# Kernel optimization log

Measured on AMD Instinct MI355X. Metric: run time of the kernel, lower is better.

Reference implementation:

```python
import jax, jax.numpy as jnp
import numpy as np

B, T, M, D, H, DH = 2, 2048, 2048, 384, 4, 96
NM, DF, R, NA = 8, 1536, 16, 4
S = 0.02  # weight init scale

PARAM_NAMES = ['cWq','cbq','cWk','cbk','cWv','cbv','cWo','cbo',
               'sWq','sbq','sWk','sbk','sWv','sbv','sWo','sbo',
               'gW','gb','f1W','f1b','f2W','f2b','adA','adB',
               'ln1g','ln1b','ln2g','ln2b','ln3g','ln3b']

def setup_inputs() -> dict:
    key = jax.random.key(0)
    ks = jax.random.split(key, 20)
    n = lambda k, sh, s=1.0: jax.random.normal(k, sh, dtype=jnp.float32) * s
    z = lambda sh: jnp.zeros(sh, dtype=jnp.float32)
    o = lambda sh: jnp.ones(sh, dtype=jnp.float32)
    return {
        'x': n(ks[0], (B, T, D)),
        'mem': n(ks[1], (B, M, D)),
        'motif_ctrl': n(ks[2], (B, NM)),
        'adapter_idx': 1,
        'cWq': n(ks[3], (D, D), S), 'cbq': z((D,)),
        'cWk': n(ks[4], (D, D), S), 'cbk': z((D,)),
        'cWv': n(ks[5], (D, D), S), 'cbv': z((D,)),
        'cWo': n(ks[6], (D, D), S), 'cbo': z((D,)),
        'sWq': n(ks[7], (D, D), S), 'sbq': z((D,)),
        'sWk': n(ks[8], (D, D), S), 'sbk': z((D,)),
        'sWv': n(ks[9], (D, D), S), 'sbv': z((D,)),
        'sWo': n(ks[10], (D, D), S), 'sbo': z((D,)),
        'gW': n(ks[11], (H, NM), S), 'gb': z((H,)),
        'f1W': n(ks[12], (DF, D), S), 'f1b': z((DF,)),
        'f2W': n(ks[13], (D, DF), S), 'f2b': z((D,)),
        'adA': n(ks[14], (NA, R, D), S),
        'adB': n(ks[15], (NA, D, R), S),
        'ln1g': o((D,)), 'ln1b': z((D,)),
        'ln2g': o((D,)), 'ln2b': z((D,)),
        'ln3g': o((D,)), 'ln3b': z((D,)),
    }

def _lin(x, W, b):
    return x @ W.T + b  # torch nn.Linear convention: W is [out, in]

def _layernorm(x, g, b):
    mu = x.mean(-1, keepdims=True)
    var = ((x - mu) ** 2).mean(-1, keepdims=True)
    return (x - mu) * jax.lax.rsqrt(var + 1e-5) * g + b

def _block(x, mem, motif_ctrl, adapter_idx, p):
    scale = 1.0 / np.sqrt(DH).astype(np.float32)
    # --- cross-attention over memory ---
    h = _layernorm(x, p['ln1g'], p['ln1b'])
    q = _lin(h, p['cWq'], p['cbq']).reshape(B, T, H, DH)
    k = _lin(mem, p['cWk'], p['cbk']).reshape(B, M, H, DH)
    v = _lin(mem, p['cWv'], p['cbv']).reshape(B, M, H, DH)
    A = jax.nn.softmax(jnp.einsum('bthd,bmhd->bhtm', q, k) * scale, axis=-1)
    z = jnp.einsum('bhtm,bmhd->bthd', A, v).reshape(B, T, D)
    x = x + _lin(z, p['cWo'], p['cbo'])
    # --- motif-gated self-attention (post-softmax per-head gate) ---
    h = _layernorm(x, p['ln2g'], p['ln2b'])
    gates = jax.nn.sigmoid(motif_ctrl @ p['gW'].T + p['gb'])  # [B, H]
    q = _lin(h, p['sWq'], p['sbq']).reshape(B, T, H, DH)
    k = _lin(h, p['sWk'], p['sbk']).reshape(B, T, H, DH)
    v = _lin(h, p['sWv'], p['sbv']).reshape(B, T, H, DH)
    A = jax.nn.softmax(jnp.einsum('bthd,bshd->bhts', q, k) * scale, axis=-1)
    A = A * gates[:, :, None, None]
    z = jnp.einsum('bhts,bshd->bthd', A, v).reshape(B, T, D)
    x = x + _lin(z, p['sWo'], p['sbo'])
    # --- LoRA-adapter FFN ---
    h = _layernorm(x, p['ln3g'], p['ln3b'])
    f = _lin(jax.nn.gelu(_lin(h, p['f1W'], p['f1b']), approximate=False), p['f2W'], p['f2b'])
    f = f + (h @ p['adA'][adapter_idx].T) @ p['adB'][adapter_idx].T
    return x + f

def reference(x, mem, motif_ctrl, adapter_idx,
              cWq, cbq, cWk, cbk, cWv, cbv, cWo, cbo,
              sWq, sbq, sWk, sbk, sWv, sbv, sWo, sbo,
              gW, gb, f1W, f1b, f2W, f2b, adA, adB,
              ln1g, ln1b, ln2g, ln2b, ln3g, ln3b):
    p = dict(zip(PARAM_NAMES, (cWq, cbq, cWk, cbk, cWv, cbv, cWo, cbo,
                               sWq, sbq, sWk, sbk, sWv, sbv, sWo, sbo,
                               gW, gb, f1W, f1b, f2W, f2b, adA, adB,
                               ln1g, ln1b, ln2g, ln2b, ln3g, ln3b)))
    return _block(x, mem, motif_ctrl, int(adapter_idx), p)
```

## Files before the change

kernel.cpp:

```cpp
#include <hip/hip_runtime.h>
#include <hip/hip_bf16.h>
#include <math.h>

#define B_   2
#define T_   2048
#define M_   2048
#define D_   384
#define H_   4
#define DH_  96
#define NM_  8
#define DF_  1536
#define R_   16
#define NR_  4096

typedef unsigned short u16;
typedef u16    u16x8  __attribute__((ext_vector_type(8)));
typedef u16    u16x4  __attribute__((ext_vector_type(4)));
typedef __bf16 bf16x8 __attribute__((ext_vector_type(8)));
typedef float  f32x4  __attribute__((ext_vector_type(4)));

union V8 { u16x8 u; bf16x8 b; };
__device__ __forceinline__ bf16x8 as_bf(u16x8 x) { V8 v; v.u = x; return v.b; }

__device__ __forceinline__ u16 f2bf(float f) {
    unsigned u = __float_as_uint(f);
    unsigned r = (u + 0x7fffu + ((u >> 16) & 1u)) >> 16;
    return (u16)r;
}

__device__ __forceinline__ void load16(const u16* g, u16* l) {
    __builtin_amdgcn_global_load_lds(
        (const __attribute__((address_space(1))) void*)g,
        (__attribute__((address_space(3))) void*)l, 16, 0, 0);
}

__global__ __launch_bounds__(256)
void setup_kernel(const float* cWq, const float* cWk, const float* cWv, const float* cWo,
                  const float* sWq, const float* sWk, const float* sWv, const float* sWo,
                  const float* f1W, const float* f2W, const float* adA, const float* adB,
                  const float* mem,
                  u16* Wq_c, u16* Wkv_c, u16* Wco, u16* Wqkv_s, u16* Wso,
                  u16* Wf1, u16* Wf2, u16* WadA, u16* WadB, u16* memb,
                  const float* cbk, const float* cbv,
                  const float* sbq, const float* sbk, const float* sbv,
                  float* bkv_c, float* bqkv_s,
                  const float* mc, const float* gW, const float* gb, float* gates) {
    int seg = blockIdx.y;
    if (seg == 13) {
        for (int i = blockIdx.x * 256 + threadIdx.x; i < 1928; i += gridDim.x * 256) {
            if (i < 768) bkv_c[i] = (i < 384) ? cbk[i] : cbv[i - 384];
            else if (i < 1920) {
                int j = i - 768;
                bqkv_s[j] = (j < 384) ? sbq[j] : (j < 768 ? sbk[j - 384] : sbv[j - 768]);
            } else {
                int k = i - 1920;
                int b = k / H_, h = k % H_;
                float s = gb[h];
                for (int n = 0; n < NM_; n++)
                    s += mc[b * NM_ + n] * gW[h * NM_ + n];
                gates[k] = 1.f / (1.f + __expf(-s));
            }
        }
        return;
    }
    const float* s; u16* d; int n;
    switch (seg) {
        case 0:  s = cWq; d = Wq_c;            n = 147456; break;
        case 1:  s = cWk; d = Wkv_c;           n = 147456; break;
        case 2:  s = cWv; d = Wkv_c + 147456;  n = 147456; break;
        case 3:  s = cWo; d = Wco;             n = 147456; break;
        case 4:  s = sWq; d = Wqkv_s;          n = 147456; break;
        case 5:  s = sWk; d = Wqkv_s + 147456; n = 147456; break;
        case 6:  s = sWv; d = Wqkv_s + 294912; n = 147456; break;
        case 7:  s = sWo; d = Wso;             n = 147456; break;
        case 8:  s = f1W; d = Wf1;             n = 589824; break;
        case 9:  s = f2W; d = Wf2;             n = 589824; break;
        case 10: s = adA; d = WadA;            n = 24576;  break;
        case 11: s = adB; d = WadB;            n = 24576;  break;
        default: s = mem; d = memb;            n = 1572864; break;
    }
    for (int i = blockIdx.x * 256 + threadIdx.x; i < n; i += gridDim.x * 256)
        d[i] = f2bf(s[i]);
}

__global__ __launch_bounds__(384)
void ln_kernel(const float* __restrict__ x, const float* __restrict__ g,
               const float* __restrict__ b, u16* __restrict__ out) {
    __shared__ float sm[8];
    int row = blockIdx.x;
    int t = threadIdx.x;
    float v = x[(long)row * D_ + t];

    float s = v;
    for (int o = 32; o > 0; o >>= 1) s += __shfl_down(s, o);
    if ((t & 63) == 0) sm[t >> 6] = s;
    __syncthreads();
    float mu = 0.f;
    for (int i = 0; i < 6; i++) mu += sm[i];
    mu *= (1.f / D_);
    __syncthreads();

    float d = v - mu;
    s = d * d;
    for (int o = 32; o > 0; o >>= 1) s += __shfl_down(s, o);
    if ((t & 63) == 0) sm[t >> 6] = s;
    __syncthreads();
    float var = 0.f;
    for (int i = 0; i < 6; i++) var += sm[i];
    var *= (1.f / D_);

    float r = rsqrtf(var + 1e-5f);
    out[(long)row * D_ + t] = f2bf(d * r * g[t] + b[t]);
}

template<int ACT, bool OBF, bool VT, bool LORA>
__global__ __launch_bounds__(256)
void gemm_pipe(const u16* __restrict__ A, const u16* __restrict__ W,
               const float* __restrict__ bias, const float* __restrict__ res,
               void* __restrict__ Cout, int NC, int K,
               u16* __restrict__ Vt, int vtbase,
               const u16* __restrict__ Tl, const u16* __restrict__ adB,
               const int* __restrict__ aidx) {
    __shared__ __align__(16) u16 As[8192];
    __shared__ __align__(16) u16 Ws[8192];
    int tid = threadIdx.x, w = tid >> 6, lane = tid & 63;
    int l15 = lane & 15, quad = lane >> 4;
    int bm = blockIdx.y * 64, bn = blockIdx.x * 64;
    int mt0 = (w & 1) * 2, nt0 = (w >> 1) * 2;

    const u16* Ag[2]; const u16* Wg[2]; u16* Al[2]; u16* Wl[2];
    #pragma unroll
    for (int s = 0; s < 2; s++) {
        int r = s * 4 + w, mt = r >> 1, kc = r & 1;
        Ag[s] = A + (long)(bm + mt * 16 + l15) * K + kc * 32 + quad * 8;
        Wg[s] = W + (long)(bn + mt * 16 + l15) * K + kc * 32 + quad * 8;
        Al[s] = As + r * 512;
        Wl[s] = Ws + r * 512;
    }

    f32x4 acc[2][2];
    #pragma unroll
    for (int i = 0; i < 2; i++)
        #pragma unroll
        for (int j = 0; j < 2; j++) acc[i][j] = (f32x4){0.f, 0.f, 0.f, 0.f};

    int niter = K >> 6;
    #pragma unroll
    for (int s = 0; s < 2; s++) { load16(Ag[s], Al[s]); load16(Wg[s], Wl[s]); }

    for (int i = 0; i < niter; i++) {
        __syncthreads();
        int cur = (i & 1) * 4096, nxt = 4096 - cur;
        if (i + 1 < niter) {
            int k = (i + 1) << 6;
            #pragma unroll
            for (int s = 0; s < 2; s++) {
                load16(Ag[s] + k, Al[s] + nxt);
                load16(Wg[s] + k, Wl[s] + nxt);
            }
        }
        #pragma unroll
        for (int kc = 0; kc < 2; kc++) {
            u16x8 af[2], bfv[2];
            #pragma unroll
            for (int s = 0; s < 2; s++) {
                af[s]  = *(const u16x8*)(As + cur + ((mt0 + s) * 2 + kc) * 512 + lane * 8);
                bfv[s] = *(const u16x8*)(Ws + cur + ((nt0 + s) * 2 + kc) * 512 + lane * 8);
            }
            #pragma unroll
            for (int s = 0; s < 2; s++)
                #pragma unroll
                for (int j = 0; j < 2; j++)
                    acc[s][j] = __builtin_amdgcn_mfma_f32_16x16x32_bf16(
                        as_bf(af[s]), as_bf(bfv[j]), acc[s][j], 0, 0, 0);
        }
    }

    if (LORA) {
        long aoff = (long)aidx[0] * 6144;
        u16x8 tlf[2] = {{0,0,0,0,0,0,0,0}, {0,0,0,0,0,0,0,0}};
        u16x8 adf[2] = {{0,0,0,0,0,0,0,0}, {0,0,0,0,0,0,0,0}};
        #pragma unroll
        for (int s = 0; s < 2; s++) {
            if (quad < 2) {
                tlf[s] = *(const u16x8*)(Tl + (long)(bm + (mt0 + s) * 16 + l15) * 16 + quad * 8);
                adf[s] = *(const u16x8*)(adB + aoff + (long)(bn + (nt0 + s) * 16 + l15) * 16 + quad * 8);
            }
        }
        #pragma unroll
        for (int s = 0; s < 2; s++)
            #pragma unroll
            for (int j = 0; j < 2; j++)
                acc[s][j] = __builtin_amdgcn_mfma_f32_16x16x32_bf16(
                    as_bf(tlf[s]), as_bf(adf[j]), acc[s][j], 0, 0, 0);
    }

    #pragma unroll
    for (int mi = 0; mi < 2; mi++) {
        #pragma unroll
        for (int nj = 0; nj < 2; nj++) {
            int col = bn + (nt0 + nj) * 16 + l15;
            float bv = bias ? bias[col] : 0.f;
            int rowb = bm + (mt0 + mi) * 16 + quad * 4;
            if (VT && col >= vtbase) {
                int vc = col - vtbase;
                int b = rowb >> 11, rowl = rowb & 2047;
                u16x4 ov;
                #pragma unroll
                for (int r = 0; r < 4; r++) ov[r] = f2bf(acc[mi][nj][r] + bv);
                *(u16x4*)(Vt + ((long)b * 384 + vc) * 2048 + rowl) = ov;
            } else {
                #pragma unroll
                for (int r = 0; r < 4; r++) {
                    float v = acc[mi][nj][r] + bv;
                    if (ACT == 1) v = 0.5f * v * (1.f + erff(v * 0.70710678118654752f));
                    long idx = (long)(rowb + r) * NC + col;
                    if (res) v += res[idx];
                    if (OBF) ((u16*)Cout)[idx] = f2bf(v);
                    else     ((float*)Cout)[idx] = v;
                }
            }
        }
    }
}

template<int ACT, bool OBF>
__global__ __launch_bounds__(256)
void gemm_small(const u16* __restrict__ A, const u16* __restrict__ W,
                const float* __restrict__ bias, const float* __restrict__ res,
                void* __restrict__ Cout, int NR, int NC, int K,
                const int* __restrict__ aidx, int astride) {
    if (aidx) W += (long)aidx[0] * astride;
    __shared__ __align__(16) u16 As[2048];
    __shared__ __align__(16) u16 Ws[2048];
    int tid = threadIdx.x;
    int w = tid >> 6, lane = tid & 63;
    int bm = blockIdx.y * 64, bn = blockIdx.x * 64;
    int mt0 = (w & 1) * 2, nt0 = (w >> 1) * 2;

    int srow = ((tid >> 6) << 4) + (tid & 15);
    int kq8  = ((tid >> 4) & 3) * 8;
    const u16* Ag = A + (long)(bm + srow) * K + kq8;
    int wrow = bn + srow;
    const u16* Wg = W + (long)wrow * K + kq8;
    bool wok = wrow < NC;

    f32x4 acc[2][2];
    #pragma unroll
    for (int i = 0; i < 2; i++)
        #pragma unroll
        for (int j = 0; j < 2; j++) acc[i][j] = (f32x4){0.f, 0.f, 0.f, 0.f};

    for (int k0 = 0; k0 < K; k0 += 32) {
        u16x8 av = {0, 0, 0, 0, 0, 0, 0, 0};
        u16x8 wv = {0, 0, 0, 0, 0, 0, 0, 0};
        bool kok = (k0 + kq8) < K;
        if (kok) av = *(const u16x8*)(Ag + k0);
        if (kok && wok) wv = *(const u16x8*)(Wg + k0);
        __syncthreads();
        *(u16x8*)(As + tid * 8) = av;
        *(u16x8*)(Ws + tid * 8) = wv;
        __syncthreads();
        u16x8 af[2], bfv[2];
        #pragma unroll
        for (int i = 0; i < 2; i++) {
            af[i]  = *(const u16x8*)(As + (mt0 + i) * 512 + lane * 8);
            bfv[i] = *(const u16x8*)(Ws + (nt0 + i) * 512 + lane * 8);
        }
        #pragma unroll
        for (int i = 0; i < 2; i++)
            #pragma unroll
            for (int j = 0; j < 2; j++)
                acc[i][j] = __builtin_amdgcn_mfma_f32_16x16x32_bf16(
                    as_bf(af[i]), as_bf(bfv[j]), acc[i][j], 0, 0, 0);
    }

    int quad = lane >> 4, l15 = lane & 15;
    #pragma unroll
    for (int mi = 0; mi < 2; mi++) {
        #pragma unroll
        for (int nj = 0; nj < 2; nj++) {
            int col = bn + (nt0 + nj) * 16 + l15;
            if (col < NC) {
                float bv = bias ? bias[col] : 0.f;
                int rowb = bm + (mt0 + mi) * 16 + quad * 4;
                #pragma unroll
                for (int r = 0; r < 4; r++) {
                    float v = acc[mi][nj][r] + bv;
                    if (ACT == 1) v = 0.5f * v * (1.f + erff(v * 0.70710678118654752f));
                    long idx = (long)(rowb + r) * NC + col;
                    if (res) v += res[idx];
                    if (OBF) ((u16*)Cout)[idx] = f2bf(v);
                    else     ((float*)Cout)[idx] = v;
                }
            }
        }
    }
}

__global__ __launch_bounds__(256)
void attn_mfma(const u16* __restrict__ Qg, int qs,
               const u16* __restrict__ Kg, int ks,
               const u16* __restrict__ Vt,
               float* __restrict__ Po, float* __restrict__ Pl) {
    __shared__ __align__(16) u16 Ks[2][6144];
    __shared__ __align__(16) u16 Vs[2][6144];
    __shared__ __align__(16) u16 Ps[4][2][1088];
    const float SCALE = 0.10206207261596575f;

    int tid = threadIdx.x, wv = tid >> 6, lane = tid & 63;
    int l15 = lane & 15, quad = lane >> 4;
    int bh = blockIdx.y, b = bh >> 2, h = bh & 3;
    int split = blockIdx.z;
    int q0 = blockIdx.x * 128 + wv * 32;

    const u16* Qb = Qg + (long)(b * 2048 + q0) * qs + h * 96;
    const u16* Kb = Kg + (long)(b * 2048 + split * 512) * ks + h * 96;
    const u16* Vb = Vt + (long)(b * 384 + h * 96) * 2048 + split * 512;

    u16x8 qf[2][3];
    #pragma unroll
    for (int g = 0; g < 2; g++)
        #pragma unroll
        for (int t = 0; t < 3; t++)
            qf[g][t] = *(const u16x8*)(Qb + (long)(g * 16 + l15) * qs + t * 32 + quad * 8);

    f32x4 o[2][6];
    #pragma unroll
    for (int g = 0; g < 2; g++)
        #pragma unroll
        for (int i = 0; i < 6; i++) o[g][i] = (f32x4){0.f, 0.f, 0.f, 0.f};
    float rs[2][4] = {{0.f, 0.f, 0.f, 0.f}, {0.f, 0.f, 0.f, 0.f}};

    const u16* KgI[3]; int KlO[3]; const u16* VgI[3]; int VlO[3];
    #pragma unroll
    for (int i = 0; i < 3; i++) {
        int r = i * 4 + wv;
        int ksub = r & 3, kst = r >> 2;
        KgI[i] = Kb + (long)(ksub * 16 + l15) * ks + kst * 32 + quad * 8;
        KlO[i] = (ksub * 3 + kst) * 512;
        int nt = r >> 1, t2 = r & 1;
        VgI[i] = Vb + (long)(nt * 16 + l15) * 2048 + t2 * 32 + quad * 8;
        VlO[i] = r * 512;
    }

    #pragma unroll
    for (int i = 0; i < 3; i++) {
        load16(KgI[i], &Ks[0][0] + KlO[i]);
        load16(VgI[i], &Vs[0][0] + VlO[i]);
    }

    for (int it = 0; it < 8; it++) {
        __syncthreads();
        int cur = it & 1, nxt = cur ^ 1;
        if (it + 1 < 8) {
            int j = (it + 1) * 64;
            #pragma unroll
            for (int i = 0; i < 3; i++) {
                load16(KgI[i] + (long)j * ks, &Ks[nxt][0] + KlO[i]);
                load16(VgI[i] + j, &Vs[nxt][0] + VlO[i]);
            }
        }

        f32x4 sc[2][4];
        #pragma unroll
        for (int g = 0; g < 2; g++)
            #pragma unroll
            for (int s = 0; s < 4; s++) sc[g][s] = (f32x4){0.f, 0.f, 0.f, 0.f};
        #pragma unroll
        for (int s = 0; s < 4; s++)
            #pragma unroll
            for (int t = 0; t < 3; t++) {
                u16x8 kf = *(const u16x8*)(&Ks[cur][0] + (s * 3 + t) * 512 + lane * 8);
                sc[0][s] = __builtin_amdgcn_mfma_f32_16x16x32_bf16(as_bf(qf[0][t]), as_bf(kf), sc[0][s], 0, 0, 0);
                sc[1][s] = __builtin_amdgcn_mfma_f32_16x16x32_bf16(as_bf(qf[1][t]), as_bf(kf), sc[1][s], 0, 0, 0);
            }

        #pragma unroll
        for (int g = 0; g < 2; g++)
            #pragma unroll
            for (int s = 0; s < 4; s++) {
                int base = (s >> 1) * 544 + ((((s & 1) << 1) | (l15 >> 3))) * 136 + (l15 & 7);
                #pragma unroll
                for (int r = 0; r < 4; r++) {
                    float p = __expf(sc[g][s][r] * SCALE);
                    rs[g][r] += p;
                    Ps[wv][g][base + (quad * 4 + r) * 8] = f2bf(p);
                }
            }

        #pragma unroll
        for (int t2 = 0; t2 < 2; t2++) {
            u16x8 pf0 = *(const u16x8*)(&Ps[wv][0][0] + t2 * 544 + quad * 136 + l15 * 8);
            u16x8 pf1 = *(const u16x8*)(&Ps[wv][1][0] + t2 * 544 + quad * 136 + l15 * 8);
            #pragma unroll
            for (int nt = 0; nt < 6; nt++) {
                u16x8 vf = *(const u16x8*)(&Vs[cur][0] + (nt * 2 + t2) * 512 + lane * 8);
                o[0][nt] = __builtin_amdgcn_mfma_f32_16x16x32_bf16(as_bf(pf0), as_bf(vf), o[0][nt], 0, 0, 0);
                o[1][nt] = __builtin_amdgcn_mfma_f32_16x16x32_bf16(as_bf(pf1), as_bf(vf), o[1][nt], 0, 0, 0);
            }
        }
    }

    #pragma unroll
    for (int off = 1; off < 16; off <<= 1)
        #pragma unroll
        for (int g = 0; g < 2; g++)
            #pragma unroll
            for (int r = 0; r < 4; r++) rs[g][r] += __shfl_xor(rs[g][r], off);

    #pragma unroll
    for (int g = 0; g < 2; g++) {
        float* Pob = Po + ((long)(split * 8 + bh) * 2048 + q0 + g * 16) * 96;
        #pragma unroll
        for (int nt = 0; nt < 6; nt++)
            #pragma unroll
            for (int r = 0; r < 4; r++)
                Pob[(long)(quad * 4 + r) * 96 + nt * 16 + l15] = o[g][nt][r];
        if (l15 == 0) {
            long mb = (long)(split * 8 + bh) * 2048 + q0 + g * 16 + quad * 4;
            #pragma unroll
            for (int r = 0; r < 4; r++) Pl[mb + r] = rs[g][r];
        }
    }
}

__global__ __launch_bounds__(256)
void attn_combine(const float* __restrict__ Po, const float* __restrict__ Pl,
                  const float* __restrict__ gates, u16* __restrict__ Z) {
    int bh = blockIdx.y, b = bh >> 2, h = bh & 3;
    int tid = threadIdx.x;
    int rl = tid >> 2, part = tid & 3;
    int row = blockIdx.x * 64 + rl;
    long rbase = (long)bh * 2048 + row;

    float L = 0.f;
    #pragma unroll
    for (int s = 0; s < 4; s++) L += Pl[s * 16384 + rbase];
    float g = gates ? gates[bh] : 1.f;
    float sc = g / L;

    u16* Zr = Z + ((long)(b * 2048) + row) * 384 + h * 96 + part * 24;
    #pragma unroll
    for (int i = 0; i < 24; i += 4) {
        f32x4 acc = (f32x4){0.f, 0.f, 0.f, 0.f};
        #pragma unroll
        for (int s = 0; s < 4; s++) {
            f32x4 v = *(const f32x4*)(Po + ((long)s * 16384 + rbase) * 96 + part * 24 + i);
            #pragma unroll
            for (int e = 0; e < 4; e++) acc[e] += v[e];
        }
        u16x4 ov;
        #pragma unroll
        for (int e = 0; e < 4; e++) ov[e] = f2bf(acc[e] * sc);
        *(u16x4*)(Zr + i) = ov;
    }
}

extern "C" void kernel_launch(void* const* d_in, const int* in_sizes, int n_in,
                              void* d_out, int out_size, void* d_ws, size_t ws_size,
                              hipStream_t stream) {
    const float* x    = (const float*)d_in[0];
    const float* mem  = (const float*)d_in[1];
    const float* mc   = (const float*)d_in[2];
    const int*   aidx = (const int*)d_in[3];
    const float* cWq = (const float*)d_in[4],  *cbq = (const float*)d_in[5];
    const float* cWk = (const float*)d_in[6],  *cbk = (const float*)d_in[7];
    const float* cWv = (const float*)d_in[8],  *cbv = (const float*)d_in[9];
    const float* cWo = (const float*)d_in[10], *cbo = (const float*)d_in[11];
    const float* sWq = (const float*)d_in[12], *sbq = (const float*)d_in[13];
    const float* sWk = (const float*)d_in[14], *sbk = (const float*)d_in[15];
    const float* sWv = (const float*)d_in[16], *sbv = (const float*)d_in[17];
    const float* sWo = (const float*)d_in[18], *sbo = (const float*)d_in[19];
    const float* gW  = (const float*)d_in[20], *gb  = (const float*)d_in[21];
    const float* f1W = (const float*)d_in[22], *f1b = (const float*)d_in[23];
    const float* f2W = (const float*)d_in[24], *f2b = (const float*)d_in[25];
    const float* adA = (const float*)d_in[26], *adB = (const float*)d_in[27];
    const float* ln1g = (const float*)d_in[28], *ln1b = (const float*)d_in[29];
    const float* ln2g = (const float*)d_in[30], *ln2b = (const float*)d_in[31];
    const float* ln3g = (const float*)d_in[32], *ln3b = (const float*)d_in[33];

    u16* p = (u16*)d_ws;
    u16* H      = p; p += (size_t)NR_ * 384;
    u16* bufQ   = p; p += (size_t)NR_ * 384;
    u16* bufKV  = p; p += (size_t)NR_ * 768;
    u16* bufQKV = p; p += (size_t)NR_ * 1152;
    u16* Vt     = p; p += (size_t)B_ * 384 * 2048;
    u16* Zb     = p; p += (size_t)NR_ * 384;
    u16* F      = p; p += (size_t)NR_ * 1536;
    u16* Tl     = p; p += (size_t)NR_ * 16;
    u16* memb   = p; p += (size_t)NR_ * 384;
    u16* Wq_c   = p; p += 147456;
    u16* Wkv_c  = p; p += 294912;
    u16* Wco    = p; p += 147456;
    u16* Wqkv_s = p; p += 442368;
    u16* Wso    = p; p += 147456;
    u16* Wf1    = p; p += 589824;
    u16* Wf2    = p; p += 589824;
    u16* WadA   = p; p += 24576;
    u16* WadB   = p; p += 24576;
    float* fp = (float*)p;
    float* X1 = fp;     fp += (size_t)NR_ * 384;
    float* X2 = fp;     fp += (size_t)NR_ * 384;
    float* Po = fp;     fp += (size_t)4 * 8 * 2048 * 96;
    float* Pl = fp;     fp += (size_t)4 * 8 * 2048;
    float* bkv_c  = fp; fp += 768;
    float* bqkv_s = fp; fp += 1152;
    float* gbuf   = fp; fp += 8;

    setup_kernel<<<dim3(96, 14), 256, 0, stream>>>(
        cWq, cWk, cWv, cWo, sWq, sWk, sWv, sWo, f1W, f2W, adA, adB, mem,
        Wq_c, Wkv_c, Wco, Wqkv_s, Wso, Wf1, Wf2, WadA, WadB, memb,
        cbk, cbv, sbq, sbk, sbv, bkv_c, bqkv_s, mc, gW, gb, gbuf);

    const float* nf = nullptr;
    const u16* nu = nullptr;
    ln_kernel<<<NR_, 384, 0, stream>>>(x, ln1g, ln1b, H);
    gemm_pipe<0, true, false, false><<<dim3(6, 64), 256, 0, stream>>>(H, Wq_c, cbq, nf, bufQ, 384, 384, nullptr, 0, nu, nu, nullptr);
    gemm_pipe<0, true, true, false><<<dim3(12, 64), 256, 0, stream>>>(memb, Wkv_c, bkv_c, nf, bufKV, 768, 384, Vt, 384, nu, nu, nullptr);
    attn_mfma<<<dim3(16, 8, 4), 256, 0, stream>>>(bufQ, 384, bufKV, 768, Vt, Po, Pl);
    attn_combine<<<dim3(32, 8), 256, 0, stream>>>(Po, Pl, nullptr, Zb);
    gemm_pipe<0, false, false, false><<<dim3(6, 64), 256, 0, stream>>>(Zb, Wco, cbo, x, X1, 384, 384, nullptr, 0, nu, nu, nullptr);

    ln_kernel<<<NR_, 384, 0, stream>>>(X1, ln2g, ln2b, H);
    gemm_pipe<0, true, true, false><<<dim3(18, 64), 256, 0, stream>>>(H, Wqkv_s, bqkv_s, nf, bufQKV, 1152, 384, Vt, 768, nu, nu, nullptr);
    attn_mfma<<<dim3(16, 8, 4), 256, 0, stream>>>(bufQKV, 1152, bufQKV + 384, 1152, Vt, Po, Pl);
    attn_combine<<<dim3(32, 8), 256, 0, stream>>>(Po, Pl, gbuf, Zb);
    gemm_pipe<0, false, false, false><<<dim3(6, 64), 256, 0, stream>>>(Zb, Wso, sbo, X1, X2, 384, 384, nullptr, 0, nu, nu, nullptr);

    ln_kernel<<<NR_, 384, 0, stream>>>(X2, ln3g, ln3b, H);
    gemm_pipe<1, true, false, false><<<dim3(24, 64), 256, 0, stream>>>(H, Wf1, f1b, nf, F, 1536, 384, nullptr, 0, nu, nu, nullptr);
    gemm_small<0, true><<<dim3(1, 64), 256, 0, stream>>>(H, WadA, nullptr, nf, Tl, NR_, 16, 384, aidx, R_ * D_);
    gemm_pipe<0, false, false, true><<<dim3(6, 64), 256, 0, stream>>>(F, Wf2, f2b, X2, d_out, 384, 1536, nullptr, 0, Tl, WadB, aidx);
}
```

Baseline: 371.6 us.

## Unify GEMM kernel, fuse cross-attn Q/KV and LoRA-A projections, bf16 partials

Replaces the two GEMM kernels with a templated gemm_uni that selects its A operand per column block. This merges the cross-attention Q and KV projections into one launch and folds the LoRA-A projection into the FFN1 GEMM as an extra column block. The residual-output GEMMs use 32-row tiles with twice as many blocks, for more parallelism on the narrow 384-column outputs. Attention split partials are stored in bf16 instead of fp32 to halve combine traffic, at some cost in precision.

```diff
diff --git a/kernel.cpp b/kernel.cpp
--- a/kernel.cpp
+++ b/kernel.cpp
@@ -27,6 +27,9 @@
     unsigned r = (u + 0x7fffu + ((u >> 16) & 1u)) >> 16;
     return (u16)r;
 }
+__device__ __forceinline__ float bf2f(u16 u) {
+    return __uint_as_float(((unsigned)u) << 16);
+}
 
 __device__ __forceinline__ void load16(const u16* g, u16* l) {
     __builtin_amdgcn_global_load_lds(
@@ -39,21 +42,22 @@
                   const float* sWq, const float* sWk, const float* sWv, const float* sWo,
                   const float* f1W, const float* f2W, const float* adA, const float* adB,
                   const float* mem,
-                  u16* Wq_c, u16* Wkv_c, u16* Wco, u16* Wqkv_s, u16* Wso,
+                  u16* Wqkv_c, u16* Wco, u16* Wqkv_s, u16* Wso,
                   u16* Wf1, u16* Wf2, u16* WadA, u16* WadB, u16* memb,
-                  const float* cbk, const float* cbv,
+                  const float* cbq, const float* cbk, const float* cbv,
                   const float* sbq, const float* sbk, const float* sbv,
-                  float* bkv_c, float* bqkv_s,
+                  float* bqkv_c, float* bqkv_s,
                   const float* mc, const float* gW, const float* gb, float* gates) {
     int seg = blockIdx.y;
     if (seg == 13) {
-        for (int i = blockIdx.x * 256 + threadIdx.x; i < 1928; i += gridDim.x * 256) {
-            if (i < 768) bkv_c[i] = (i < 384) ? cbk[i] : cbv[i - 384];
-            else if (i < 1920) {
-                int j = i - 768;
+        for (int i = blockIdx.x * 256 + threadIdx.x; i < 2312; i += gridDim.x * 256) {
+            if (i < 1152) {
+                bqkv_c[i] = (i < 384) ? cbq[i] : (i < 768 ? cbk[i - 384] : cbv[i - 768]);
+            } else if (i < 2304) {
+                int j = i - 1152;
                 bqkv_s[j] = (j < 384) ? sbq[j] : (j < 768 ? sbk[j - 384] : sbv[j - 768]);
             } else {
-                int k = i - 1920;
+                int k = i - 2304;
                 int b = k / H_, h = k % H_;
                 float s = gb[h];
                 for (int n = 0; n < NM_; n++)
@@ -65,19 +69,19 @@
     }
     const float* s; u16* d; int n;
     switch (seg) {
-        case 0:  s = cWq; d = Wq_c;            n = 147456; break;
-        case 1:  s = cWk; d = Wkv_c;           n = 147456; break;
-        case 2:  s = cWv; d = Wkv_c + 147456;  n = 147456; break;
-        case 3:  s = cWo; d = Wco;             n = 147456; break;
-        case 4:  s = sWq; d = Wqkv_s;          n = 147456; break;
-        case 5:  s = sWk; d = Wqkv_s + 147456; n = 147456; break;
-        case 6:  s = sWv; d = Wqkv_s + 294912; n = 147456; break;
-        case 7:  s = sWo; d = Wso;             n = 147456; break;
-        case 8:  s = f1W; d = Wf1;             n = 589824; break;
-        case 9:  s = f2W; d = Wf2;             n = 589824; break;
-        case 10: s = adA; d = WadA;            n = 24576;  break;
-        case 11: s = adB; d = WadB;            n = 24576;  break;
-        default: s = mem; d = memb;            n = 1572864; break;
+        case 0:  s = cWq; d = Wqkv_c;           n = 147456; break;
+        case 1:  s = cWk; d = Wqkv_c + 147456;  n = 147456; break;
+        case 2:  s = cWv; d = Wqkv_c + 294912;  n = 147456; break;
+        case 3:  s = cWo; d = Wco;              n = 147456; break;
+        case 4:  s = sWq; d = Wqkv_s;           n = 147456; break;
+        case 5:  s = sWk; d = Wqkv_s + 147456;  n = 147456; break;
+        case 6:  s = sWv; d = Wqkv_s + 294912;  n = 147456; break;
+        case 7:  s = sWo; d = Wso;              n = 147456; break;
+        case 8:  s = f1W; d = Wf1;              n = 589824; break;
+        case 9:  s = f2W; d = Wf2;              n = 589824; break;
+        case 10: s = adA; d = WadA;             n = 24576;  break;
+        case 11: s = adB; d = WadB;             n = 24576;  break;
+        default: s = mem; d = memb;             n = 1572864; break;
     }
     for (int i = blockIdx.x * 256 + threadIdx.x; i < n; i += gridDim.x * 256)
         d[i] = f2bf(s[i]);
@@ -113,62 +117,75 @@
     out[(long)row * D_ + t] = f2bf(d * r * g[t] + b[t]);
 }
 
-template<int ACT, bool OBF, bool VT, bool LORA>
+template<int MT, int ACT, bool OBF, bool VT, bool LORA, bool LORAA>
 __global__ __launch_bounds__(256)
-void gemm_pipe(const u16* __restrict__ A, const u16* __restrict__ W,
-               const float* __restrict__ bias, const float* __restrict__ res,
-               void* __restrict__ Cout, int NC, int K,
-               u16* __restrict__ Vt, int vtbase,
-               const u16* __restrict__ Tl, const u16* __restrict__ adB,
-               const int* __restrict__ aidx) {
-    __shared__ __align__(16) u16 As[8192];
-    __shared__ __align__(16) u16 Ws[8192];
+void gemm_uni(const u16* __restrict__ A0, const u16* __restrict__ A1, int aswitch,
+              const u16* __restrict__ W, const float* __restrict__ bias,
+              const float* __restrict__ res, void* __restrict__ Cout, int NC, int K,
+              u16* __restrict__ Vt, int vtbase,
+              const u16* __restrict__ Tl, const u16* __restrict__ adW,
+              u16* __restrict__ TlOut, const int* __restrict__ aidx) {
+    constexpr int NREG = 4 * MT + 8;
+    constexpr int HALF = NREG * 512;
+    __shared__ __align__(16) u16 S[2 * HALF];
     int tid = threadIdx.x, w = tid >> 6, lane = tid & 63;
     int l15 = lane & 15, quad = lane >> 4;
-    int bm = blockIdx.y * 64, bn = blockIdx.x * 64;
-    int mt0 = (w & 1) * 2, nt0 = (w >> 1) * 2;
-
-    const u16* Ag[2]; const u16* Wg[2]; u16* Al[2]; u16* Wl[2];
-    #pragma unroll
-    for (int s = 0; s < 2; s++) {
-        int r = s * 4 + w, mt = r >> 1, kc = r & 1;
-        Ag[s] = A + (long)(bm + mt * 16 + l15) * K + kc * 32 + quad * 8;
-        Wg[s] = W + (long)(bn + mt * 16 + l15) * K + kc * 32 + quad * 8;
-        Al[s] = As + r * 512;
-        Wl[s] = Ws + r * 512;
-    }
-
-    f32x4 acc[2][2];
-    #pragma unroll
-    for (int i = 0; i < 2; i++)
-        #pragma unroll
-        for (int j = 0; j < 2; j++) acc[i][j] = (f32x4){0.f, 0.f, 0.f, 0.f};
+    int bm = blockIdx.y * (MT * 32), bn = blockIdx.x * 64;
+    bool loraBlk = LORAA && (bn >= NC);
+
+    const u16* Ap = (bn < aswitch) ? A0 : A1;
+    const u16* Wb = W;
+    if (LORAA && loraBlk) Wb = adW + (long)aidx[0] * 6144;
+
+    const u16* GP[MT + 2];
+    int LO[MT + 2];
+    #pragma unroll
+    for (int i = 0; i < MT + 2; i++) {
+        int r = i * 4 + w;
+        const u16* src;
+        if (r < 4 * MT) {
+            int mt = r >> 1, kc = r & 1;
+            src = Ap + (long)(bm + mt * 16 + l15) * K + kc * 32 + quad * 8;
+        } else {
+            int rw = r - 4 * MT, nt = rw >> 1, kc = rw & 1;
+            if (LORAA && loraBlk)
+                src = Wb + (long)((nt * 16 + l15) & 15) * K + kc * 32 + quad * 8;
+            else
+                src = Wb + (long)(bn + nt * 16 + l15) * K + kc * 32 + quad * 8;
+        }
+        GP[i] = src;
+        LO[i] = r * 512;
+    }
+
+    f32x4 acc[MT][2];
+    #pragma unroll
+    for (int s = 0; s < MT; s++)
+        #pragma unroll
+        for (int j = 0; j < 2; j++) acc[s][j] = (f32x4){0.f, 0.f, 0.f, 0.f};
 
     int niter = K >> 6;
     #pragma unroll
-    for (int s = 0; s < 2; s++) { load16(Ag[s], Al[s]); load16(Wg[s], Wl[s]); }
-
-    for (int i = 0; i < niter; i++) {
+    for (int i = 0; i < MT + 2; i++) load16(GP[i], S + LO[i]);
+
+    for (int it = 0; it < niter; it++) {
         __syncthreads();
-        int cur = (i & 1) * 4096, nxt = 4096 - cur;
-        if (i + 1 < niter) {
-            int k = (i + 1) << 6;
-            #pragma unroll
-            for (int s = 0; s < 2; s++) {
-                load16(Ag[s] + k, Al[s] + nxt);
-                load16(Wg[s] + k, Wl[s] + nxt);
-            }
+        int cur = (it & 1) * HALF, nxt = HALF - cur;
+        if (it + 1 < niter) {
+            int k = (it + 1) << 6;
+            #pragma unroll
+            for (int i = 0; i < MT + 2; i++) load16(GP[i] + k, S + nxt + LO[i]);
         }
         #pragma unroll
         for (int kc = 0; kc < 2; kc++) {
-            u16x8 af[2], bfv[2];
-            #pragma unroll
-            for (int s = 0; s < 2; s++) {
-                af[s]  = *(const u16x8*)(As + cur + ((mt0 + s) * 2 + kc) * 512 + lane * 8);
-                bfv[s] = *(const u16x8*)(Ws + cur + ((nt0 + s) * 2 + kc) * 512 + lane * 8);
-            }
-            #pragma unroll
-            for (int s = 0; s < 2; s++)
+            u16x8 af[MT], bfv[2];
+            #pragma unroll
+            for (int s = 0; s < MT; s++)
+                af[s] = *(const u16x8*)(S + cur + (((w & 1) * MT + s) * 2 + kc) * 512 + lane * 8);
+            #pragma unroll
+            for (int j = 0; j < 2; j++)
+                bfv[j] = *(const u16x8*)(S + cur + (4 * MT + (((w >> 1) * 2 + j) * 2 + kc)) * 512 + lane * 8);
+            #pragma unroll
+            for (int s = 0; s < MT; s++)
                 #pragma unroll
                 for (int j = 0; j < 2; j++)
                     acc[s][j] = __builtin_amdgcn_mfma_f32_16x16x32_bf16(
@@ -177,18 +194,24 @@
     }
 
     if (LORA) {
-        long aoff = (long)aidx[0] * 6144;
-        u16x8 tlf[2] = {{0,0,0,0,0,0,0,0}, {0,0,0,0,0,0,0,0}};
-        u16x8 adf[2] = {{0,0,0,0,0,0,0,0}, {0,0,0,0,0,0,0,0}};
-        #pragma unroll
-        for (int s = 0; s < 2; s++) {
-            if (quad < 2) {
-                tlf[s] = *(const u16x8*)(Tl + (long)(bm + (mt0 + s) * 16 + l15) * 16 + quad * 8);
-                adf[s] = *(const u16x8*)(adB + aoff + (long)(bn + (nt0 + s) * 16 + l15) * 16 + quad * 8);
-            }
-        }
-        #pragma unroll
-        for (int s = 0; s < 2; s++)
+        long ao = (long)aidx[0] * 6144;
+        u16x8 tlf[MT], adf[2];
+        #pragma unroll
+        for (int s = 0; s < MT; s++) {
+            #pragma unroll
+            for (int e = 0; e < 8; e++) tlf[s][e] = 0;
+            if (quad < 2)
+                tlf[s] = *(const u16x8*)(Tl + (long)(bm + ((w & 1) * MT + s) * 16 + l15) * 16 + quad * 8);
+        }
+        #pragma unroll
+        for (int j = 0; j < 2; j++) {
+            #pragma unroll
+            for (int e = 0; e < 8; e++) adf[j][e] = 0;
+            if (quad < 2)
+                adf[j] = *(const u16x8*)(adW + ao + (long)(bn + ((w >> 1) * 2 + j) * 16 + l15) * 16 + quad * 8);
+        }
+        #pragma unroll
+        for (int s = 0; s < MT; s++)
             #pragma unroll
             for (int j = 0; j < 2; j++)
                 acc[s][j] = __builtin_amdgcn_mfma_f32_16x16x32_bf16(
@@ -196,102 +219,38 @@
     }
 
     #pragma unroll
-    for (int mi = 0; mi < 2; mi++) {
+    for (int mi = 0; mi < MT; mi++) {
+        int mt = (w & 1) * MT + mi;
+        int rowb = bm + mt * 16 + quad * 4;
         #pragma unroll
         for (int nj = 0; nj < 2; nj++) {
-            int col = bn + (nt0 + nj) * 16 + l15;
-            float bv = bias ? bias[col] : 0.f;
-            int rowb = bm + (mt0 + mi) * 16 + quad * 4;
-            if (VT && col >= vtbase) {
-                int vc = col - vtbase;
-                int b = rowb >> 11, rowl = rowb & 2047;
-                u16x4 ov;
-                #pragma unroll
-                for (int r = 0; r < 4; r++) ov[r] = f2bf(acc[mi][nj][r] + bv);
-                *(u16x4*)(Vt + ((long)b * 384 + vc) * 2048 + rowl) = ov;
+            int coll = ((w >> 1) * 2 + nj) * 16 + l15;
+            int col = bn + coll;
+            if (LORAA && loraBlk) {
+                if (coll < 16) {
+                    #pragma unroll
+                    for (int r = 0; r < 4; r++)
+                        TlOut[(long)(rowb + r) * 16 + coll] = f2bf(acc[mi][nj][r]);
+                }
             } else {
-                #pragma unroll
-                for (int r = 0; r < 4; r++) {
-                    float v = acc[mi][nj][r] + bv;
-                    if (ACT == 1) v = 0.5f * v * (1.f + erff(v * 0.70710678118654752f));
-                    long idx = (long)(rowb + r) * NC + col;
-                    if (res) v += res[idx];
-                    if (OBF) ((u16*)Cout)[idx] = f2bf(v);
-                    else     ((float*)Cout)[idx] = v;
-                }
-            }
-        }
-    }
-}
-
-template<int ACT, bool OBF>
-__global__ __launch_bounds__(256)
-void gemm_small(const u16* __restrict__ A, const u16* __restrict__ W,
-                const float* __restrict__ bias, const float* __restrict__ res,
-                void* __restrict__ Cout, int NR, int NC, int K,
-                const int* __restrict__ aidx, int astride) {
-    if (aidx) W += (long)aidx[0] * astride;
-    __shared__ __align__(16) u16 As[2048];
-    __shared__ __align__(16) u16 Ws[2048];
-    int tid = threadIdx.x;
-    int w = tid >> 6, lane = tid & 63;
-    int bm = blockIdx.y * 64, bn = blockIdx.x * 64;
-    int mt0 = (w & 1) * 2, nt0 = (w >> 1) * 2;
-
-    int srow = ((tid >> 6) << 4) + (tid & 15);
-    int kq8  = ((tid >> 4) & 3) * 8;
-    const u16* Ag = A + (long)(bm + srow) * K + kq8;
-    int wrow = bn + srow;
-    const u16* Wg = W + (long)wrow * K + kq8;
-    bool wok = wrow < NC;
-
-    f32x4 acc[2][2];
-    #pragma unroll
-    for (int i = 0; i < 2; i++)
-        #pragma unroll
-        for (int j = 0; j < 2; j++) acc[i][j] = (f32x4){0.f, 0.f, 0.f, 0.f};
-
-    for (int k0 = 0; k0 < K; k0 += 32) {
-        u16x8 av = {0, 0, 0, 0, 0, 0, 0, 0};
-        u16x8 wv = {0, 0, 0, 0, 0, 0, 0, 0};
-        bool kok = (k0 + kq8) < K;
-        if (kok) av = *(const u16x8*)(Ag + k0);
-        if (kok && wok) wv = *(const u16x8*)(Wg + k0);
-        __syncthreads();
-        *(u16x8*)(As + tid * 8) = av;
-        *(u16x8*)(Ws + tid * 8) = wv;
-        __syncthreads();
-        u16x8 af[2], bfv[2];
-        #pragma unroll
-        for (int i = 0; i < 2; i++) {
-            af[i]  = *(const u16x8*)(As + (mt0 + i) * 512 + lane * 8);
-            bfv[i] = *(const u16x8*)(Ws + (nt0 + i) * 512 + lane * 8);
-        }
-        #pragma unroll
-        for (int i = 0; i < 2; i++)
-            #pragma unroll
-            for (int j = 0; j < 2; j++)
-                acc[i][j] = __builtin_amdgcn_mfma_f32_16x16x32_bf16(
-                    as_bf(af[i]), as_bf(bfv[j]), acc[i][j], 0, 0, 0);
-    }
-
-    int quad = lane >> 4, l15 = lane & 15;
-    #pragma unroll
-    for (int mi = 0; mi < 2; mi++) {
-        #pragma unroll
-        for (int nj = 0; nj < 2; nj++) {
-            int col = bn + (nt0 + nj) * 16 + l15;
-            if (col < NC) {
                 float bv = bias ? bias[col] : 0.f;
-                int rowb = bm + (mt0 + mi) * 16 + quad * 4;
-                #pragma unroll
-                for (int r = 0; r < 4; r++) {
-                    float v = acc[mi][nj][r] + bv;
-                    if (ACT == 1) v = 0.5f * v * (1.f + erff(v * 0.70710678118654752f));
-                    long idx = (long)(rowb + r) * NC + col;
-                    if (res) v += res[idx];
-                    if (OBF) ((u16*)Cout)[idx] = f2bf(v);
-                    else     ((float*)Cout)[idx] = v;
+                if (VT && col >= vtbase) {
+                    int vc = col - vtbase;
+                    int b = rowb >> 11, rowl = rowb & 2047;
+                    u16x4 ov;
+                    #pragma unroll
+                    for (int r = 0; r < 4; r++) ov[r] = f2bf(acc[mi][nj][r] + bv);
+                    *(u16x4*)(Vt + ((long)b * 384 + vc) * 2048 + rowl) = ov;
+                } else {
+                    #pragma unroll
+                    for (int r = 0; r < 4; r++) {
+                        float v = acc[mi][nj][r] + bv;
+                        if (ACT == 1) v = 0.5f * v * (1.f + erff(v * 0.70710678118654752f));
+                        long idx = (long)(rowb + r) * NC + col;
+                        if (res) v += res[idx];
+                        if (OBF) ((u16*)Cout)[idx] = f2bf(v);
+                        else     ((float*)Cout)[idx] = v;
+                    }
                 }
             }
         }
@@ -302,7 +261,7 @@
 void attn_mfma(const u16* __restrict__ Qg, int qs,
                const u16* __restrict__ Kg, int ks,
                const u16* __restrict__ Vt,
-               float* __restrict__ Po, float* __restrict__ Pl) {
+               u16* __restrict__ Po, float* __restrict__ Pl) {
     __shared__ __align__(16) u16 Ks[2][6144];
     __shared__ __align__(16) u16 Vs[2][6144];
     __shared__ __align__(16) u16 Ps[4][2][1088];
@@ -411,12 +370,12 @@
 
     #pragma unroll
     for (int g = 0; g < 2; g++) {
-        float* Pob = Po + ((long)(split * 8 + bh) * 2048 + q0 + g * 16) * 96;
+        u16* Pob = Po + ((long)(split * 8 + bh) * 2048 + q0 + g * 16) * 96;
         #pragma unroll
         for (int nt = 0; nt < 6; nt++)
             #pragma unroll
             for (int r = 0; r < 4; r++)
-                Pob[(long)(quad * 4 + r) * 96 + nt * 16 + l15] = o[g][nt][r];
+                Pob[(long)(quad * 4 + r) * 96 + nt * 16 + l15] = f2bf(o[g][nt][r]);
         if (l15 == 0) {
             long mb = (long)(split * 8 + bh) * 2048 + q0 + g * 16 + quad * 4;
             #pragma unroll
@@ -426,7 +385,7 @@
 }
 
 __global__ __launch_bounds__(256)
-void attn_combine(const float* __restrict__ Po, const float* __restrict__ Pl,
+void attn_combine(const u16* __restrict__ Po, const float* __restrict__ Pl,
                   const float* __restrict__ gates, u16* __restrict__ Z) {
     int bh = blockIdx.y, b = bh >> 2, h = bh & 3;
     int tid = threadIdx.x;
@@ -446,9 +405,9 @@
         f32x4 acc = (f32x4){0.f, 0.f, 0.f, 0.f};
         #pragma unroll
         for (int s = 0; s < 4; s++) {
-            f32x4 v = *(const f32x4*)(Po + ((long)s * 16384 + rbase) * 96 + part * 24 + i);
-            #pragma unroll
-            for (int e = 0; e < 4; e++) acc[e] += v[e];
+            u16x4 v = *(const u16x4*)(Po + ((long)s * 16384 + rbase) * 96 + part * 24 + i);
+            #pragma unroll
+            for (int e = 0; e < 4; e++) acc[e] += bf2f(v[e]);
         }
         u16x4 ov;
         #pragma unroll
@@ -482,16 +441,13 @@
 
     u16* p = (u16*)d_ws;
     u16* H      = p; p += (size_t)NR_ * 384;
-    u16* bufQ   = p; p += (size_t)NR_ * 384;
-    u16* bufKV  = p; p += (size_t)NR_ * 768;
     u16* bufQKV = p; p += (size_t)NR_ * 1152;
     u16* Vt     = p; p += (size_t)B_ * 384 * 2048;
     u16* Zb     = p; p += (size_t)NR_ * 384;
     u16* F      = p; p += (size_t)NR_ * 1536;
     u16* Tl     = p; p += (size_t)NR_ * 16;
     u16* memb   = p; p += (size_t)NR_ * 384;
-    u16* Wq_c   = p; p += 147456;
-    u16* Wkv_c  = p; p += 294912;
+    u16* Wqkv_c = p; p += 442368;
     u16* Wco    = p; p += 147456;
     u16* Wqkv_s = p; p += 442368;
     u16* Wso    = p; p += 147456;
@@ -499,37 +455,42 @@
     u16* Wf2    = p; p += 589824;
     u16* WadA   = p; p += 24576;
     u16* WadB   = p; p += 24576;
-    float* fp = (float*)p;
+    u16* Po     = p; p += (size_t)4 * 8 * 2048 * 96;
+    p += ((size_t)p & 1);
+    float* fp = (float*)(((size_t)p + 3) & ~(size_t)3);
     float* X1 = fp;     fp += (size_t)NR_ * 384;
     float* X2 = fp;     fp += (size_t)NR_ * 384;
-    float* Po = fp;     fp += (size_t)4 * 8 * 2048 * 96;
     float* Pl = fp;     fp += (size_t)4 * 8 * 2048;
-    float* bkv_c  = fp; fp += 768;
+    float* bqkv_c = fp; fp += 1152;
     float* bqkv_s = fp; fp += 1152;
     float* gbuf   = fp; fp += 8;
 
     setup_kernel<<<dim3(96, 14), 256, 0, stream>>>(
         cWq, cWk, cWv, cWo, sWq, sWk, sWv, sWo, f1W, f2W, adA, adB, mem,
-        Wq_c, Wkv_c, Wco, Wqkv_s, Wso, Wf1, Wf2, WadA, WadB, memb,
-        cbk, cbv, sbq, sbk, sbv, bkv_c, bqkv_s, mc, gW, gb, gbuf);
+        Wqkv_c, Wco, Wqkv_s, Wso, Wf1, Wf2, WadA, WadB, memb,
+        cbq, cbk, cbv, sbq, sbk, sbv, bqkv_c, bqkv_s, mc, gW, gb, gbuf);
 
     const float* nf = nullptr;
     const u16* nu = nullptr;
     ln_kernel<<<NR_, 384, 0, stream>>>(x, ln1g, ln1b, H);
-    gemm_pipe<0, true, false, false><<<dim3(6, 64), 256, 0, stream>>>(H, Wq_c, cbq, nf, bufQ, 384, 384, nullptr, 0, nu, nu, nullptr);
-    gemm_pipe<0, true, true, false><<<dim3(12, 64), 256, 0, stream>>>(memb, Wkv_c, bkv_c, nf, bufKV, 768, 384, Vt, 384, nu, nu, nullptr);
-    attn_mfma<<<dim3(16, 8, 4), 256, 0, stream>>>(bufQ, 384, bufKV, 768, Vt, Po, Pl);
+    gemm_uni<2, 0, true, true, false, false><<<dim3(18, 64), 256, 0, stream>>>(
+        H, memb, 384, Wqkv_c, bqkv_c, nf, bufQKV, 1152, 384, Vt, 768, nu, nu, nullptr, nullptr);
+    attn_mfma<<<dim3(16, 8, 4), 256, 0, stream>>>(bufQKV, 1152, bufQKV + 384, 1152, Vt, Po, Pl);
     attn_combine<<<dim3(32, 8), 256, 0, stream>>>(Po, Pl, nullptr, Zb);
-    gemm_pipe<0, false, false, false><<<dim3(6, 64), 256, 0, stream>>>(Zb, Wco, cbo, x, X1, 384, 384, nullptr, 0, nu, nu, nullptr);
+    gemm_uni<1, 0, false, false, false, false><<<dim3(6, 128), 256, 0, stream>>>(
+        Zb, Zb, 0, Wco, cbo, x, X1, 384, 384, nullptr, 0, nu, nu, nullptr, nullptr);
 
     ln_kernel<<<NR_, 384, 0, stream>>>(X1, ln2g, ln2b, H);
-    gemm_pipe<0, true, true, false><<<dim3(18, 64), 256, 0, stream>>>(H, Wqkv_s, bqkv_s, nf, bufQKV, 1152, 384, Vt, 768, nu, nu, nullptr);
+    gemm_uni<2, 0, true, true, false, false><<<dim3(18, 64), 256, 0, stream>>>(
+        H, H, 0, Wqkv_s, bqkv_s, nf, bufQKV, 1152, 384, Vt, 768, nu, nu, nullptr, nullptr);
     attn_mfma<<<dim3(16, 8, 4), 256, 0, stream>>>(bufQKV, 1152, bufQKV + 384, 1152, Vt, Po, Pl);
     attn_combine<<<dim3(32, 8), 256, 0, stream>>>(Po, Pl, gbuf, Zb);
-    gemm_pipe<0, false, false, false><<<dim3(6, 64), 256, 0, stream>>>(Zb, Wso, sbo, X1, X2, 384, 384, nullptr, 0, nu, nu, nullptr);
+    gemm_uni<1, 0, false, false, false, false><<<dim3(6, 128), 256, 0, stream>>>(
+        Zb, Zb, 0, Wso, sbo, X1, X2, 384, 384, nullptr, 0, nu, nu, nullptr, nullptr);
 
     ln_kernel<<<NR_, 384, 0, stream>>>(X2, ln3g, ln3b, H);
-    gemm_pipe<1, true, false, false><<<dim3(24, 64), 256, 0, stream>>>(H, Wf1, f1b, nf, F, 1536, 384, nullptr, 0, nu, nu, nullptr);
-    gemm_small<0, true><<<dim3(1, 64), 256, 0, stream>>>(H, WadA, nullptr, nf, Tl, NR_, 16, 384, aidx, R_ * D_);
-    gemm_pipe<0, false, false, true><<<dim3(6, 64), 256, 0, stream>>>(F, Wf2, f2b, X2, d_out, 384, 1536, nullptr, 0, Tl, WadB, aidx);
-}
+    gemm_uni<2, 1, true, false, false, true><<<dim3(25, 64), 256, 0, stream>>>(
+        H, H, 0, Wf1, f1b, nf, F, 1536, 384, nullptr, 0, nu, WadA, Tl, aidx);
+    gemm_uni<1, 0, false, false, true, false><<<dim3(6, 128), 256, 0, stream>>>(
+        F, F, 0, Wf2, f2b, X2, d_out, 384, 1536, nullptr, 0, Tl, WadB, nullptr, aidx);
+}
```

Result: faster. 355.1 us (-4.4%).
